# Performance work log

Hardware: AMD Instinct MI355X
Metric: run time of the kernel (lower is better)

The kernel has to match this reference:

```python
import jax, jax.numpy as jnp
import numpy as np

SWIGLU_LIMIT = 7.0
NUM_EXPERTS = 8
HIDDEN = 2880
INTER = 2880
TOKENS = 512
TOP_K = 4
W_SCALE = 0.02  # realistic init scale; keeps activations off the clamp rails


def setup_inputs() -> dict:
    key = jax.random.key(0)
    k_t, k_idx, k_gu, k_gub, k_d, k_db = jax.random.split(key, 6)
    t = jax.random.normal(k_t, (TOKENS, HIDDEN), dtype=jnp.float32)
    expert_indices = jax.random.randint(k_idx, (TOKENS, TOP_K), 0, NUM_EXPERTS)
    gate_up_proj = jax.random.normal(k_gu, (NUM_EXPERTS, 2 * INTER, HIDDEN), dtype=jnp.float32) * W_SCALE
    gate_up_proj_bias = jax.random.normal(k_gub, (NUM_EXPERTS, 2 * INTER), dtype=jnp.float32) * W_SCALE
    down_proj = jax.random.normal(k_d, (NUM_EXPERTS, HIDDEN, INTER), dtype=jnp.float32) * W_SCALE
    down_proj_bias = jax.random.normal(k_db, (NUM_EXPERTS, HIDDEN), dtype=jnp.float32) * W_SCALE
    return {
        "t": t,
        "expert_indices": expert_indices,
        "gate_up_proj": gate_up_proj,
        "gate_up_proj_bias": gate_up_proj_bias,
        "down_proj": down_proj,
        "down_proj_bias": down_proj_bias,
    }


def reference(t, expert_indices, gate_up_proj, gate_up_proj_bias, down_proj, down_proj_bias):
    # Same math as torch's gate_up_proj[expert_indices] einsum, but we avoid
    # materializing [B,K,2I,H] duplicated weights: compute all experts then gather.
    # h_all: [B, E, 2I]
    h_all = jnp.einsum('eck,bk->bec', gate_up_proj, t)
    # gather per (token, selected expert): [B, K, 2I]
    h = jnp.take_along_axis(h_all, expert_indices[:, :, None], axis=1)
    h = h + gate_up_proj_bias[expert_indices]
    x_glu = jnp.minimum(h[..., ::2], SWIGLU_LIMIT)
    x_lin = jnp.clip(h[..., 1::2], -SWIGLU_LIMIT, SWIGLU_LIMIT)
    out_glu = x_glu * jax.nn.sigmoid(1.702 * x_glu)
    u = out_glu * (x_lin + 1.0)  # [B, K, I]
    # down-proj for all experts then gather: y_all [B, K, E, H]
    y_all = jnp.einsum('ehi,bki->bkeh', down_proj, u)
    y = jnp.take_along_axis(y_all, expert_indices[:, :, None, None], axis=2)[:, :, 0, :]
    y = y + down_proj_bias[expert_indices]
    return y  # [B, K, H]
```

## Files before the change

### kernel.cpp

```cpp
#include <hip/hip_runtime.h>
#include <hip/hip_bf16.h>

#define HIDDEN   2880
#define INTER    2880
#define NEXP     8
#define GUP_ROWS 5760
#define NPAIR    2048

#define NKT   45
#define BM    320
#define BN    96
#define TILE_B  40960
#define PLANE_B 5120

#define MAXTILES 15
#define IMG_BYTES ((size_t)MAXTILES * NKT * TILE_B)

#define ABUF 40960
#define BBUF 24576

using bf16x8 = __attribute__((ext_vector_type(8))) short;
using f32x4  = __attribute__((ext_vector_type(4))) float;

typedef const __attribute__((address_space(1))) unsigned GBuf;
typedef __attribute__((address_space(3))) unsigned LBuf;

__device__ __forceinline__ void gl2lds(const void* g, void* l) {
  __builtin_amdgcn_global_load_lds((GBuf*)g, (LBuf*)l, 16, 0, 0);
}
__device__ __forceinline__ void wait_vm8() {
  asm volatile("s_waitcnt vmcnt(8)" ::: "memory");
  __builtin_amdgcn_sched_barrier(0);
}
__device__ __forceinline__ void wait_vm0() {
  asm volatile("s_waitcnt vmcnt(0)" ::: "memory");
  __builtin_amdgcn_sched_barrier(0);
}
__device__ __forceinline__ void barrier() {
  __builtin_amdgcn_sched_barrier(0);
  __builtin_amdgcn_s_barrier();
  __builtin_amdgcn_sched_barrier(0);
}

__device__ __forceinline__ unsigned cvt2bf(float a, float b) {
  union { __hip_bfloat16 h; unsigned short s; } x, y;
  x.h = __float2bfloat16(a);
  y.h = __float2bfloat16(b);
  return (unsigned)x.s | ((unsigned)y.s << 16);
}
__device__ __forceinline__ bf16x8 cvt8(const float4& lo, const float4& hi) {
  union { bf16x8 v; unsigned u[4]; } r;
  r.u[0] = cvt2bf(lo.x, lo.y);
  r.u[1] = cvt2bf(lo.z, lo.w);
  r.u[2] = cvt2bf(hi.x, hi.y);
  r.u[3] = cvt2bf(hi.z, hi.w);
  return r.v;
}

__global__ void route_count(const int* __restrict__ eidx, int* __restrict__ meta) {
  __shared__ int cnt[NEXP];
  int t = threadIdx.x;
  if (t < NEXP) cnt[t] = 0;
  __syncthreads();
  for (int a = t; a < NPAIR; a += 256) atomicAdd(&cnt[eidx[a]], 1);
  __syncthreads();
  if (t == 0) {
    int off = 0, toff = 0;
    for (int e = 0; e < NEXP; ++e) {
      meta[e] = cnt[e];
      meta[8 + e] = off;
      meta[16 + e] = off;
      meta[24 + e] = toff;
      off += cnt[e];
      toff += (cnt[e] + BM - 1) / BM;
    }
  }
}

__global__ void route_scatter(const int* __restrict__ eidx, int* __restrict__ meta,
                              int* __restrict__ list) {
  int a = blockIdx.x * 256 + threadIdx.x;
  int e = eidx[a];
  int pos = atomicAdd(&meta[16 + e], 1);
  list[pos] = a;
}

__global__ void gather_a(const float* __restrict__ t, const int* __restrict__ eidx,
                         const int* __restrict__ meta, const int* __restrict__ list,
                         char* __restrict__ atile) {
  const int i = blockIdx.x;
  const int a = list[i];
  const int e = eidx[a];
  const int r = i - meta[8 + e];
  const int tile = meta[24 + e] + r / BM;
  const int row = r % BM;
  const float* src = t + (size_t)(a >> 2) * HIDDEN;
  for (int ch = threadIdx.x; ch < HIDDEN / 8; ch += 256) {
    int kt = ch >> 3, p = ch & 7;
    const float4* s = (const float4*)(src + ch * 8);
    float4 v0 = s[0], v1 = s[1];
    uint4 w;
    w.x = cvt2bf(v0.x, v0.y); w.y = cvt2bf(v0.z, v0.w);
    w.z = cvt2bf(v1.x, v1.y); w.w = cvt2bf(v1.z, v1.w);
    *(uint4*)(atile + (size_t)(tile * NKT + kt) * TILE_B + p * PLANE_B + row * 16) = w;
  }
}

template<int NCOLS_TOT, bool SWIGLU>
__global__ __launch_bounds__(512, 2)
void gemm_core(const char* __restrict__ aimg,
               const float* __restrict__ wgt,
               const float* __restrict__ wbias,
               const int* __restrict__ meta,
               const int* __restrict__ list,
               char* __restrict__ uimg,
               float* __restrict__ out)
{
  const int e = blockIdx.x, nt = blockIdx.y, mt = blockIdx.z;
  const int n_e = meta[e];
  const int m0 = mt * BM;
  if (m0 >= n_e) return;
  const int tile = meta[24 + e] + mt;

  __shared__ __align__(16) char lds[2 * ABUF + 2 * BBUF];
  char* ldsB = lds + 2 * ABUF;

  const int tid = threadIdx.x, lane = tid & 63, wid = tid >> 6;
  const int wm = wid >> 1, wn = wid & 1;
  const int kq = lane >> 4, l15 = lane & 15;

  const char* aSrcBase = aimg + (size_t)tile * NKT * TILE_B;
  const char* srcA[5];
  int dstA[5];
  #pragma unroll
  for (int j = 0; j < 5; ++j) {
    int c = wid * 5 + j;
    srcA[j] = aSrcBase + c * 1024 + lane * 16;
    dstA[j] = c * 1024;
  }
  const char* srcB[3];
  int dstB[3];
  #pragma unroll
  for (int j = 0; j < 3; ++j) {
    int cb = wid * 3 + j;
    int col = nt * BN + cb * 4 + (lane >> 4);
    int s16 = lane & 15;
    int swz = (((s16 >> 1) ^ (col & 7)) << 5) | ((s16 & 1) << 4);
    srcB[j] = (const char*)wgt + ((size_t)(e * NCOLS_TOT + col) * HIDDEN) * 4 + swz;
    dstB[j] = cb * 1024;
  }

  auto STAGE = [&](int kt, int buf) {
    #pragma unroll
    for (int j = 0; j < 5; ++j)
      gl2lds(srcA[j] + (size_t)kt * TILE_B, lds + buf * ABUF + dstA[j]);
    #pragma unroll
    for (int j = 0; j < 3; ++j)
      gl2lds(srcB[j] + (size_t)kt * 256, ldsB + buf * BBUF + dstB[j]);
  };

  f32x4 acc[5][3];
  #pragma unroll
  for (int fm = 0; fm < 5; ++fm)
    #pragma unroll
    for (int fn = 0; fn < 3; ++fn)
      acc[fm][fn] = f32x4{0.f, 0.f, 0.f, 0.f};

  auto COMP = [&](int buf) {
    const char* aT = lds + buf * ABUF;
    const char* bT = ldsB + buf * BBUF;
    #pragma unroll
    for (int s = 0; s < 2; ++s) {
      const char* aB = aT + (s * 4 + kq) * PLANE_B + (wm * 80 + l15) * 16;
      bf16x8 af[5], bf[3];
      #pragma unroll
      for (int fm = 0; fm < 5; ++fm) af[fm] = *(const bf16x8*)(aB + fm * 256);
      #pragma unroll
      for (int fn = 0; fn < 3; ++fn) {
        int col = wn * 48 + fn * 16 + l15;
        int slot = ((s * 4 + kq) ^ (col & 7)) << 5;
        const char* cp = bT + col * 256 + slot;
        float4 lo = *(const float4*)cp;
        float4 hi = *(const float4*)(cp + 16);
        bf[fn] = cvt8(lo, hi);
      }
      #pragma unroll
      for (int fm = 0; fm < 5; ++fm)
        #pragma unroll
        for (int fn = 0; fn < 3; ++fn)
          acc[fm][fn] = __builtin_amdgcn_mfma_f32_16x16x32_bf16(af[fm], bf[fn], acc[fm][fn], 0, 0, 0);
    }
  };

  STAGE(0, 0);
  for (int kt = 0; kt < NKT; ++kt) {
    if (kt + 1 < NKT) { STAGE(kt + 1, (kt + 1) & 1); wait_vm8(); }
    else wait_vm0();
    barrier();
    COMP(kt & 1);
    barrier();
  }

  if (SWIGLU) {
    #pragma unroll
    for (int fm = 0; fm < 5; ++fm) {
      #pragma unroll
      for (int fn = 0; fn < 3; ++fn) {
        const int colg = nt * BN + wn * 48 + fn * 16 + l15;
        const float bias = wbias[e * NCOLS_TOT + colg];
        #pragma unroll
        for (int j = 0; j < 4; ++j) {
          float h = acc[fm][fn][j] + bias;
          float other = __shfl_xor(h, 1, 64);
          int rowin = wm * 80 + fm * 16 + kq * 4 + j;
          if (!(lane & 1) && (m0 + rowin) < n_e) {
            float xg = fminf(h, 7.0f);
            float xl = fminf(fmaxf(other, -7.0f), 7.0f);
            float og = xg / (1.0f + __expf(-1.702f * xg));
            float uv = og * (xl + 1.0f);
            int uc = colg >> 1;
            int kt2 = uc >> 6, p2 = (uc >> 3) & 7;
            *(__hip_bfloat16*)(uimg + (size_t)(tile * NKT + kt2) * TILE_B +
                p2 * PLANE_B + rowin * 16 + (uc & 7) * 2) = __float2bfloat16(uv);
          }
        }
      }
    }
  } else {
    const int base = meta[8 + e];
    #pragma unroll
    for (int fm = 0; fm < 5; ++fm) {
      #pragma unroll
      for (int j = 0; j < 4; ++j) {
        int rL = m0 + wm * 80 + fm * 16 + kq * 4 + j;
        int aidx = (rL < n_e) ? list[base + rL] : -1;
        #pragma unroll
        for (int fn = 0; fn < 3; ++fn) {
          int col = nt * BN + wn * 48 + fn * 16 + l15;
          if (aidx >= 0)
            out[(size_t)aidx * HIDDEN + col] = acc[fm][fn][j] + wbias[e * NCOLS_TOT + col];
        }
      }
    }
  }
}

extern "C" void kernel_launch(void* const* d_in, const int* in_sizes, int n_in,
                              void* d_out, int out_size, void* d_ws, size_t ws_size,
                              hipStream_t stream) {
  const float* t     = (const float*)d_in[0];
  const int*   eidx  = (const int*)d_in[1];
  const float* gup   = (const float*)d_in[2];
  const float* gub   = (const float*)d_in[3];
  const float* dwn   = (const float*)d_in[4];
  const float* dbias = (const float*)d_in[5];
  float* out = (float*)d_out;

  char* ws = (char*)d_ws;
  char* atile = ws;
  char* utile = ws + IMG_BYTES;
  int* meta = (int*)(ws + 2 * IMG_BYTES);
  int* list = meta + 32;

  route_count<<<1, 256, 0, stream>>>(eidx, meta);
  route_scatter<<<NPAIR / 256, 256, 0, stream>>>(eidx, meta, list);
  gather_a<<<NPAIR, 256, 0, stream>>>(t, eidx, meta, list, atile);

  dim3 g1(NEXP, GUP_ROWS / BN, 2);
  gemm_core<GUP_ROWS, true><<<g1, 512, 0, stream>>>(atile, gup, gub, meta, list, utile, out);

  dim3 g2(NEXP, HIDDEN / BN, 2);
  gemm_core<HIDDEN, false><<<g2, 512, 0, stream>>>(utile, dwn, dbias, meta, list, nullptr, out);
}
```

Measured before the change: 334.5 us.

## Widen GEMM N tile to 160 and skip A loads for empty rows

Raises the per-block N tile from 96 to 160 columns, with a 5x5 MFMA fragment grid per wave and a larger B LDS buffer, so each A tile staged into LDS is reused across more weight columns. The A-staging layout is reorganised so each wave loads one K-plane, which lets partial M tiles skip loading 64-row chunks that hold no valid rows. The vmcnt wait is adjusted to match the number of loads issued. In exchange the kernel uses more accumulator registers and more LDS, which can lower occupancy under the existing launch bounds of 2 blocks per CU.

```diff
diff --git a/kernel.cpp b/kernel.cpp
--- a/kernel.cpp
+++ b/kernel.cpp
@@ -9,7 +9,7 @@
 
 #define NKT   45
 #define BM    320
-#define BN    96
+#define BN    160
 #define TILE_B  40960
 #define PLANE_B 5120
 
@@ -17,7 +17,7 @@
 #define IMG_BYTES ((size_t)MAXTILES * NKT * TILE_B)
 
 #define ABUF 40960
-#define BBUF 24576
+#define BBUF 40960
 
 using bf16x8 = __attribute__((ext_vector_type(8))) short;
 using f32x4  = __attribute__((ext_vector_type(4))) float;
@@ -28,14 +28,8 @@
 __device__ __forceinline__ void gl2lds(const void* g, void* l) {
   __builtin_amdgcn_global_load_lds((GBuf*)g, (LBuf*)l, 16, 0, 0);
 }
-__device__ __forceinline__ void wait_vm8() {
-  asm volatile("s_waitcnt vmcnt(8)" ::: "memory");
-  __builtin_amdgcn_sched_barrier(0);
-}
-__device__ __forceinline__ void wait_vm0() {
-  asm volatile("s_waitcnt vmcnt(0)" ::: "memory");
-  __builtin_amdgcn_sched_barrier(0);
-}
+#define WAITVM(N) { asm volatile("s_waitcnt vmcnt(" #N ")" ::: "memory"); \
+                    __builtin_amdgcn_sched_barrier(0); }
 __device__ __forceinline__ void barrier() {
   __builtin_amdgcn_sched_barrier(0);
   __builtin_amdgcn_s_barrier();
@@ -121,6 +115,8 @@
   const int m0 = mt * BM;
   if (m0 >= n_e) return;
   const int tile = meta[24 + e] + mt;
+  int rows = n_e - m0; if (rows > BM) rows = BM;
+  const int V = (rows + 63) >> 6;
 
   __shared__ __align__(16) char lds[2 * ABUF + 2 * BBUF];
   char* ldsB = lds + 2 * ABUF;
@@ -134,15 +130,14 @@
   int dstA[5];
   #pragma unroll
   for (int j = 0; j < 5; ++j) {
-    int c = wid * 5 + j;
-    srcA[j] = aSrcBase + c * 1024 + lane * 16;
-    dstA[j] = c * 1024;
-  }
-  const char* srcB[3];
-  int dstB[3];
+    srcA[j] = aSrcBase + wid * PLANE_B + j * 1024 + lane * 16;
+    dstA[j] = wid * PLANE_B + j * 1024;
+  }
+  const char* srcB[5];
+  int dstB[5];
   #pragma unroll
-  for (int j = 0; j < 3; ++j) {
-    int cb = wid * 3 + j;
+  for (int j = 0; j < 5; ++j) {
+    int cb = wid * 5 + j;
     int col = nt * BN + cb * 4 + (lane >> 4);
     int s16 = lane & 15;
     int swz = (((s16 >> 1) ^ (col & 7)) << 5) | ((s16 & 1) << 4);
@@ -153,17 +148,18 @@
   auto STAGE = [&](int kt, int buf) {
     #pragma unroll
     for (int j = 0; j < 5; ++j)
-      gl2lds(srcA[j] + (size_t)kt * TILE_B, lds + buf * ABUF + dstA[j]);
-    #pragma unroll
-    for (int j = 0; j < 3; ++j)
+      if (j < V)
+        gl2lds(srcA[j] + (size_t)kt * TILE_B, lds + buf * ABUF + dstA[j]);
+    #pragma unroll
+    for (int j = 0; j < 5; ++j)
       gl2lds(srcB[j] + (size_t)kt * 256, ldsB + buf * BBUF + dstB[j]);
   };
 
-  f32x4 acc[5][3];
+  f32x4 acc[5][5];
   #pragma unroll
   for (int fm = 0; fm < 5; ++fm)
     #pragma unroll
-    for (int fn = 0; fn < 3; ++fn)
+    for (int fn = 0; fn < 5; ++fn)
       acc[fm][fn] = f32x4{0.f, 0.f, 0.f, 0.f};
 
   auto COMP = [&](int buf) {
@@ -172,12 +168,12 @@
     #pragma unroll
     for (int s = 0; s < 2; ++s) {
       const char* aB = aT + (s * 4 + kq) * PLANE_B + (wm * 80 + l15) * 16;
-      bf16x8 af[5], bf[3];
+      bf16x8 af[5], bf[5];
       #pragma unroll
       for (int fm = 0; fm < 5; ++fm) af[fm] = *(const bf16x8*)(aB + fm * 256);
       #pragma unroll
-      for (int fn = 0; fn < 3; ++fn) {
-        int col = wn * 48 + fn * 16 + l15;
+      for (int fn = 0; fn < 5; ++fn) {
+        int col = wn * 80 + fn * 16 + l15;
         int slot = ((s * 4 + kq) ^ (col & 7)) << 5;
         const char* cp = bT + col * 256 + slot;
         float4 lo = *(const float4*)cp;
@@ -187,15 +183,21 @@
       #pragma unroll
       for (int fm = 0; fm < 5; ++fm)
         #pragma unroll
-        for (int fn = 0; fn < 3; ++fn)
+        for (int fn = 0; fn < 5; ++fn)
           acc[fm][fn] = __builtin_amdgcn_mfma_f32_16x16x32_bf16(af[fm], bf[fn], acc[fm][fn], 0, 0, 0);
     }
   };
 
   STAGE(0, 0);
   for (int kt = 0; kt < NKT; ++kt) {
-    if (kt + 1 < NKT) { STAGE(kt + 1, (kt + 1) & 1); wait_vm8(); }
-    else wait_vm0();
+    if (kt + 1 < NKT) {
+      STAGE(kt + 1, (kt + 1) & 1);
+      if      (V == 5) WAITVM(10)
+      else if (V == 4) WAITVM(9)
+      else if (V == 3) WAITVM(8)
+      else if (V == 2) WAITVM(7)
+      else             WAITVM(6)
+    } else WAITVM(0)
     barrier();
     COMP(kt & 1);
     barrier();
@@ -205,15 +207,15 @@
     #pragma unroll
     for (int fm = 0; fm < 5; ++fm) {
       #pragma unroll
-      for (int fn = 0; fn < 3; ++fn) {
-        const int colg = nt * BN + wn * 48 + fn * 16 + l15;
+      for (int fn = 0; fn < 5; ++fn) {
+        const int colg = nt * BN + wn * 80 + fn * 16 + l15;
         const float bias = wbias[e * NCOLS_TOT + colg];
         #pragma unroll
         for (int j = 0; j < 4; ++j) {
           float h = acc[fm][fn][j] + bias;
           float other = __shfl_xor(h, 1, 64);
           int rowin = wm * 80 + fm * 16 + kq * 4 + j;
-          if (!(lane & 1) && (m0 + rowin) < n_e) {
+          if (!(lane & 1) && rowin < rows) {
             float xg = fminf(h, 7.0f);
             float xl = fminf(fmaxf(other, -7.0f), 7.0f);
             float og = xg / (1.0f + __expf(-1.702f * xg));
@@ -232,11 +234,11 @@
     for (int fm = 0; fm < 5; ++fm) {
       #pragma unroll
       for (int j = 0; j < 4; ++j) {
-        int rL = m0 + wm * 80 + fm * 16 + kq * 4 + j;
-        int aidx = (rL < n_e) ? list[base + rL] : -1;
+        int rin = wm * 80 + fm * 16 + kq * 4 + j;
+        int aidx = (rin < rows) ? list[base + m0 + rin] : -1;
         #pragma unroll
-        for (int fn = 0; fn < 3; ++fn) {
-          int col = nt * BN + wn * 48 + fn * 16 + l15;
+        for (int fn = 0; fn < 5; ++fn) {
+          int col = nt * BN + wn * 80 + fn * 16 + l15;
           if (aidx >= 0)
             out[(size_t)aidx * HIDDEN + col] = acc[fm][fn][j] + wbias[e * NCOLS_TOT + col];
         }
```

Measured after the change: 442.5 us. 1.32x slower.

## Halve K-tile depth and deepen GEMM prefetch pipeline to five LDS buffers

Applied to the files above, without the earlier changes.

Shrinks each K step from 64 to 32 elements, doubling the number of K tiles, and rearranges the A image layout to match. The LDS ring grows from double buffering to five buffers with four stages in flight, each wave issuing four loads per stage. The aim is to hide global-memory latency on the FP32 weight stream with deeper prefetch. In exchange there are twice as many barriers per tile, more LDS per block (160KB), which may cap occupancy at one block per CU, and a changed B swizzle.

```diff
diff --git a/kernel.cpp b/kernel.cpp
--- a/kernel.cpp
+++ b/kernel.cpp
@@ -7,17 +7,16 @@
 #define GUP_ROWS 5760
 #define NPAIR    2048
 
-#define NKT   45
+#define NKT   90
 #define BM    320
 #define BN    96
-#define TILE_B  40960
-#define PLANE_B 5120
-
-#define MAXTILES 15
-#define IMG_BYTES ((size_t)MAXTILES * NKT * TILE_B)
-
-#define ABUF 40960
-#define BBUF 24576
+#define ATILE 20480
+#define APLANE 5120
+#define BUFSZ  32768
+#define NBUF   5
+
+#define MAXTILES 14
+#define IMG_BYTES ((size_t)MAXTILES * NKT * ATILE)
 
 using bf16x8 = __attribute__((ext_vector_type(8))) short;
 using f32x4  = __attribute__((ext_vector_type(4))) float;
@@ -28,14 +27,8 @@
 __device__ __forceinline__ void gl2lds(const void* g, void* l) {
   __builtin_amdgcn_global_load_lds((GBuf*)g, (LBuf*)l, 16, 0, 0);
 }
-__device__ __forceinline__ void wait_vm8() {
-  asm volatile("s_waitcnt vmcnt(8)" ::: "memory");
-  __builtin_amdgcn_sched_barrier(0);
-}
-__device__ __forceinline__ void wait_vm0() {
-  asm volatile("s_waitcnt vmcnt(0)" ::: "memory");
-  __builtin_amdgcn_sched_barrier(0);
-}
+#define WAITVM(N) { asm volatile("s_waitcnt vmcnt(" #N ")" ::: "memory"); \
+                    __builtin_amdgcn_sched_barrier(0); }
 __device__ __forceinline__ void barrier() {
   __builtin_amdgcn_sched_barrier(0);
   __builtin_amdgcn_s_barrier();
@@ -96,13 +89,13 @@
   const int row = r % BM;
   const float* src = t + (size_t)(a >> 2) * HIDDEN;
   for (int ch = threadIdx.x; ch < HIDDEN / 8; ch += 256) {
-    int kt = ch >> 3, p = ch & 7;
+    int kt = ch >> 2, kq = ch & 3;
     const float4* s = (const float4*)(src + ch * 8);
     float4 v0 = s[0], v1 = s[1];
     uint4 w;
     w.x = cvt2bf(v0.x, v0.y); w.y = cvt2bf(v0.z, v0.w);
     w.z = cvt2bf(v1.x, v1.y); w.w = cvt2bf(v1.z, v1.w);
-    *(uint4*)(atile + (size_t)(tile * NKT + kt) * TILE_B + p * PLANE_B + row * 16) = w;
+    *(uint4*)(atile + (size_t)(tile * NKT + kt) * ATILE + kq * APLANE + row * 16) = w;
   }
 }
 
@@ -121,42 +114,40 @@
   const int m0 = mt * BM;
   if (m0 >= n_e) return;
   const int tile = meta[24 + e] + mt;
-
-  __shared__ __align__(16) char lds[2 * ABUF + 2 * BBUF];
-  char* ldsB = lds + 2 * ABUF;
+  int rows = n_e - m0; if (rows > BM) rows = BM;
+
+  __shared__ __align__(16) char lds[NBUF * BUFSZ];
 
   const int tid = threadIdx.x, lane = tid & 63, wid = tid >> 6;
   const int wm = wid >> 1, wn = wid & 1;
   const int kq = lane >> 4, l15 = lane & 15;
 
-  const char* aSrcBase = aimg + (size_t)tile * NKT * TILE_B;
-  const char* srcA[5];
-  int dstA[5];
+  const char* aSrc = aimg + (size_t)tile * NKT * ATILE;
+
+  const char* srcP[4]; int dstOff[4]; int strd[4];
   #pragma unroll
-  for (int j = 0; j < 5; ++j) {
-    int c = wid * 5 + j;
-    srcA[j] = aSrcBase + c * 1024 + lane * 16;
-    dstA[j] = c * 1024;
-  }
-  const char* srcB[3];
-  int dstB[3];
-  #pragma unroll
-  for (int j = 0; j < 3; ++j) {
-    int cb = wid * 3 + j;
-    int col = nt * BN + cb * 4 + (lane >> 4);
-    int s16 = lane & 15;
-    int swz = (((s16 >> 1) ^ (col & 7)) << 5) | ((s16 & 1) << 4);
-    srcB[j] = (const char*)wgt + ((size_t)(e * NCOLS_TOT + col) * HIDDEN) * 4 + swz;
-    dstB[j] = cb * 1024;
-  }
-
-  auto STAGE = [&](int kt, int buf) {
-    #pragma unroll
-    for (int j = 0; j < 5; ++j)
-      gl2lds(srcA[j] + (size_t)kt * TILE_B, lds + buf * ABUF + dstA[j]);
-    #pragma unroll
-    for (int j = 0; j < 3; ++j)
-      gl2lds(srcB[j] + (size_t)kt * 256, ldsB + buf * BBUF + dstB[j]);
+  for (int j = 0; j < 4; ++j) {
+    int c = wid * 4 + j;
+    if (c < 20) {
+      srcP[j] = aSrc + c * 1024 + lane * 16;
+      strd[j] = ATILE;
+      dstOff[j] = c * 1024;
+    } else {
+      int cb = c - 20;
+      int col = nt * BN + cb * 8 + (lane >> 3);
+      int g = (lane & 7) >> 1, h = lane & 1;
+      srcP[j] = (const char*)wgt + (size_t)(e * NCOLS_TOT + col) * (HIDDEN * 4)
+                + (((g ^ (col & 3)) << 5) | (h << 4));
+      strd[j] = 128;
+      dstOff[j] = 20480 + cb * 1024;
+    }
+  }
+
+  auto STAGE = [&](int kt, int b) {
+    char* dst = lds + b * BUFSZ;
+    #pragma unroll
+    for (int j = 0; j < 4; ++j)
+      gl2lds(srcP[j] + (size_t)kt * strd[j], dst + dstOff[j]);
   };
 
   f32x4 acc[5][3];
@@ -166,40 +157,42 @@
     for (int fn = 0; fn < 3; ++fn)
       acc[fm][fn] = f32x4{0.f, 0.f, 0.f, 0.f};
 
-  auto COMP = [&](int buf) {
-    const char* aT = lds + buf * ABUF;
-    const char* bT = ldsB + buf * BBUF;
-    #pragma unroll
-    for (int s = 0; s < 2; ++s) {
-      const char* aB = aT + (s * 4 + kq) * PLANE_B + (wm * 80 + l15) * 16;
-      bf16x8 af[5], bf[3];
+  auto COMP = [&](int b) {
+    const char* base = lds + b * BUFSZ;
+    const char* aB = base + kq * APLANE + (wm * 80 + l15) * 16;
+    bf16x8 af[5], bf[3];
+    #pragma unroll
+    for (int fm = 0; fm < 5; ++fm) af[fm] = *(const bf16x8*)(aB + fm * 256);
+    #pragma unroll
+    for (int fn = 0; fn < 3; ++fn) {
+      int col = wn * 48 + fn * 16 + l15;
+      const char* cp = base + 20480 + col * 128 + ((kq ^ (col & 3)) << 5);
+      float4 lo = *(const float4*)cp;
+      float4 hi = *(const float4*)(cp + 16);
+      bf[fn] = cvt8(lo, hi);
+    }
+    #pragma unroll
+    for (int fm = 0; fm < 5; ++fm)
       #pragma unroll
-      for (int fm = 0; fm < 5; ++fm) af[fm] = *(const bf16x8*)(aB + fm * 256);
-      #pragma unroll
-      for (int fn = 0; fn < 3; ++fn) {
-        int col = wn * 48 + fn * 16 + l15;
-        int slot = ((s * 4 + kq) ^ (col & 7)) << 5;
-        const char* cp = bT + col * 256 + slot;
-        float4 lo = *(const float4*)cp;
-        float4 hi = *(const float4*)(cp + 16);
-        bf[fn] = cvt8(lo, hi);
-      }
-      #pragma unroll
-      for (int fm = 0; fm < 5; ++fm)
-        #pragma unroll
-        for (int fn = 0; fn < 3; ++fn)
-          acc[fm][fn] = __builtin_amdgcn_mfma_f32_16x16x32_bf16(af[fm], bf[fn], acc[fm][fn], 0, 0, 0);
-    }
+      for (int fn = 0; fn < 3; ++fn)
+        acc[fm][fn] = __builtin_amdgcn_mfma_f32_16x16x32_bf16(af[fm], bf[fn], acc[fm][fn], 0, 0, 0);
   };
 
-  STAGE(0, 0);
-  for (int kt = 0; kt < NKT; ++kt) {
-    if (kt + 1 < NKT) { STAGE(kt + 1, (kt + 1) & 1); wait_vm8(); }
-    else wait_vm0();
+  STAGE(0, 0); STAGE(1, 1); STAGE(2, 2); STAGE(3, 3);
+  int b = 0, sb = 4;
+  for (int kt = 0; kt < NKT - 4; ++kt) {
+    WAITVM(12);
     barrier();
-    COMP(kt & 1);
+    COMP(b);
     barrier();
-  }
+    STAGE(kt + 4, sb);
+    b  = (b  == 4) ? 0 : b  + 1;
+    sb = (sb == 4) ? 0 : sb + 1;
+  }
+  WAITVM(12); barrier(); COMP(b); barrier(); b = (b == 4) ? 0 : b + 1;
+  WAITVM(8);  barrier(); COMP(b); barrier(); b = (b == 4) ? 0 : b + 1;
+  WAITVM(4);  barrier(); COMP(b); barrier(); b = (b == 4) ? 0 : b + 1;
+  WAITVM(0);  barrier(); COMP(b);
 
   if (SWIGLU) {
     #pragma unroll
@@ -213,15 +206,15 @@
           float h = acc[fm][fn][j] + bias;
           float other = __shfl_xor(h, 1, 64);
           int rowin = wm * 80 + fm * 16 + kq * 4 + j;
-          if (!(lane & 1) && (m0 + rowin) < n_e) {
+          if (!(lane & 1) && rowin < rows) {
             float xg = fminf(h, 7.0f);
             float xl = fminf(fmaxf(other, -7.0f), 7.0f);
             float og = xg / (1.0f + __expf(-1.702f * xg));
             float uv = og * (xl + 1.0f);
             int uc = colg >> 1;
-            int kt2 = uc >> 6, p2 = (uc >> 3) & 7;
-            *(__hip_bfloat16*)(uimg + (size_t)(tile * NKT + kt2) * TILE_B +
-                p2 * PLANE_B + rowin * 16 + (uc & 7) * 2) = __float2bfloat16(uv);
+            int kt2 = uc >> 5, kq2 = (uc >> 3) & 3;
+            *(__hip_bfloat16*)(uimg + (size_t)(tile * NKT + kt2) * ATILE +
+                kq2 * APLANE + rowin * 16 + (uc & 7) * 2) = __float2bfloat16(uv);
           }
         }
       }
@@ -232,8 +225,8 @@
     for (int fm = 0; fm < 5; ++fm) {
       #pragma unroll
       for (int j = 0; j < 4; ++j) {
-        int rL = m0 + wm * 80 + fm * 16 + kq * 4 + j;
-        int aidx = (rL < n_e) ? list[base + rL] : -1;
+        int rin = wm * 80 + fm * 16 + kq * 4 + j;
+        int aidx = (rin < rows) ? list[base + m0 + rin] : -1;
         #pragma unroll
         for (int fn = 0; fn < 3; ++fn) {
           int col = nt * BN + wn * 48 + fn * 16 + l15;
```

Result: slower. 402.8 us (+20.4%).
